# Optimization experiments

Measured on AMD Instinct MI355X. Metric: run time of the kernel, lower is better.

Reference implementation:

```python
import jax, jax.numpy as jnp
import numpy as np

N, E, D_IN, D, L = 50000, 100000, 78, 768, 5
BN_EPS = 1e-5


def setup_inputs() -> dict:
    key = jax.random.key(0)
    ks = jax.random.split(key, 8)
    s_in = 1.0 / np.sqrt(D_IN)
    s_d = 1.0 / np.sqrt(D)
    return {
        "x": jax.random.normal(ks[0], (N, D_IN), dtype=jnp.float32),
        "edge_index": jax.random.randint(ks[1], (2, E), 0, N, dtype=jnp.int32),
        "in_w": jax.random.normal(ks[2], (D_IN, D), dtype=jnp.float32) * s_in,
        "in_b": jnp.zeros((D,), jnp.float32),
        "conv_w": jax.random.normal(ks[3], (L, D, D), dtype=jnp.float32) * s_d,
        "conv_b": jnp.zeros((L, D), jnp.float32),
        "bn_g": jnp.ones((L, D), jnp.float32),
        "bn_b": jnp.zeros((L, D), jnp.float32),
        "out_w": jax.random.normal(ks[4], (D, D), dtype=jnp.float32) * s_d,
        "out_b": jnp.zeros((D,), jnp.float32),
    }


def reference(x, edge_index, in_w, in_b, conv_w, conv_b, bn_g, bn_b, out_w, out_b):
    src, dst = edge_index[0], edge_index[1]
    # GCN symmetric normalization with self-loops: deg over dst (col), +1 for self-loop
    deg = jax.ops.segment_sum(jnp.ones((E,), x.dtype), dst, num_segments=N) + 1.0
    dinv = jax.lax.rsqrt(deg)                      # deg >= 1, always finite
    edge_norm = (dinv[src] * dinv[dst])[:, None]   # [E, 1]
    self_norm = (dinv * dinv)[:, None]             # [N, 1] self-loop coefficient

    h = x @ in_w + in_b                            # input_proj -> [N, D]
    for l in range(L):
        xw = h @ conv_w[l]                         # GCNConv linear
        agg = jax.ops.segment_sum(xw[src] * edge_norm, dst, num_segments=N)
        agg = agg + xw * self_norm + conv_b[l]     # self-loop message + bias
        # BatchNorm1d (training mode: batch stats, biased variance)
        mu = jnp.mean(agg, axis=0)
        var = jnp.mean(jnp.square(agg - mu), axis=0)
        hn = (agg - mu) * jax.lax.rsqrt(var + BN_EPS) * bn_g[l] + bn_b[l]
        h = h + jax.nn.relu(hn)                    # residual (drop_ratio=0)
    return h @ out_w + out_b
```

## Files before the change

kernel.cpp:

```cpp
#include <hip/hip_runtime.h>
#include <hip/hip_bf16.h>
#include <stdint.h>

#define NN 50000
#define EE 100000
#define DD 768
#define MP 50176
#define KIN 96
#define SCB 196

typedef _Float16 half_t;
typedef __attribute__((ext_vector_type(8))) _Float16 v8h;
typedef __attribute__((ext_vector_type(4))) float v4f;

__device__ __forceinline__ void gload16(const half_t* g, half_t* l){
  __builtin_amdgcn_global_load_lds(
      (const __attribute__((address_space(1))) unsigned int*)(g),
      (__attribute__((address_space(3))) unsigned int*)(l),
      16, 0, 0);
}

template<int MODE>
__global__ __launch_bounds__(512, 2)
void gemm256_k(const half_t* __restrict__ A,
               const half_t* __restrict__ Bt,
               int K,
               const float* __restrict__ bias,
               float* __restrict__ o32,
               half_t* __restrict__ o16)
{
  __shared__ __align__(16) half_t lds[3*16384];

  const int nwg = gridDim.x;
  const int q = nwg >> 3, r = nwg & 7;
  const int xcd = blockIdx.x & 7, ii = blockIdx.x >> 3;
  const int L = (xcd < r ? xcd*(q+1) : r*(q+1) + (xcd-r)*q) + ii;
  const int rowb = L / 3, colb = L - rowb*3;
  const int m0 = rowb*256, n0 = colb*256;

  const int t = threadIdx.x, l = t&63, w = t>>6;
  const int wm = w>>2, wn = w&3;

  v4f acc[8][4];
  #pragma unroll
  for (int i=0;i<8;++i)
    #pragma unroll
    for (int j=0;j<4;++j){ v4f z = {0.f,0.f,0.f,0.f}; acc[i][j]=z; }

  const int strip = w*2;
  const int srow  = strip*16 + (l>>2);
  const int sch   = ((l&3) ^ ((l>>2)&3))*8;
  const half_t* Asrc = A  + (size_t)(m0 + srow)*K + sch;
  const half_t* Bsrc = Bt + (size_t)(n0 + srow)*K + sch;

  auto STAGE = [&](int kt2, int b){
    half_t* Ab = lds + b*16384;
    half_t* Bb = Ab + 8192;
    const int ko = kt2*32;
    gload16(Asrc + ko,                    Ab + strip*512);
    gload16(Bsrc + ko,                    Bb + strip*512);
    gload16(Asrc + ko + (size_t)16*K,     Ab + strip*512 + 512);
    gload16(Bsrc + ko + (size_t)16*K,     Bb + strip*512 + 512);
  };

  const int nkt = K/32;
  STAGE(0,0); STAGE(1,1); STAGE(2,2);

  const int ra = l&15;
  const int pc = ((l>>4) ^ (l&3))*8;

  int cb = 0;
  for (int kt=0; kt<nkt; ++kt){
    if (kt < nkt-2)      asm volatile("s_waitcnt vmcnt(8)" ::: "memory");
    else if (kt==nkt-2)  asm volatile("s_waitcnt vmcnt(4)" ::: "memory");
    else                 asm volatile("s_waitcnt vmcnt(0)" ::: "memory");
    __builtin_amdgcn_s_barrier();
    asm volatile("" ::: "memory");

    const half_t* Ab = lds + cb*16384;
    const half_t* Bb = Ab + 8192;
    v8h af[8], bf[4];
    #pragma unroll
    for (int n=0;n<4;++n)
      bf[n] = *(const v8h*)(Bb + (wn*64 + n*16 + ra)*32 + pc);
    #pragma unroll
    for (int m=0;m<8;++m)
      af[m] = *(const v8h*)(Ab + (wm*128 + m*16 + ra)*32 + pc);

    __builtin_amdgcn_s_setprio(1);
    #pragma unroll
    for (int m=0;m<8;++m)
      #pragma unroll
      for (int n=0;n<4;++n)
        acc[m][n] = __builtin_amdgcn_mfma_f32_16x16x32_f16(af[m], bf[n], acc[m][n], 0,0,0);
    __builtin_amdgcn_s_setprio(0);

    asm volatile("" ::: "memory");
    __builtin_amdgcn_s_barrier();
    asm volatile("" ::: "memory");

    if (kt+3 < nkt) STAGE(kt+3, cb);
    cb = (cb==2) ? 0 : cb+1;
  }

  if (MODE==2){
    float bv[4];
    #pragma unroll
    for (int n=0;n<4;++n) bv[n] = bias[n0 + wn*64 + n*16 + ra];
    #pragma unroll
    for (int m=0;m<8;++m){
      #pragma unroll
      for (int rr=0;rr<4;++rr){
        int row = m0 + wm*128 + m*16 + (l>>4)*4 + rr;
        if (row >= NN) continue;
        #pragma unroll
        for (int n=0;n<4;++n){
          int col = n0 + wn*64 + n*16 + ra;
          o32[(size_t)row*DD + col] = acc[m][n][rr] + bv[n];
        }
      }
    }
  } else {
    #pragma unroll
    for (int p=0;p<2;++p){
      __syncthreads();
      if (wm==p){
        #pragma unroll
        for (int m=0;m<8;++m)
          #pragma unroll
          for (int rr=0;rr<4;++rr){
            int rw = m*16 + (l>>4)*4 + rr;
            #pragma unroll
            for (int n=0;n<4;++n){
              int col = wn*64 + n*16 + ra;
              lds[rw*256 + (col ^ ((rw&15)<<3))] = (half_t)acc[m][n][rr];
            }
          }
      }
      __syncthreads();
      #pragma unroll
      for (int g=0; g<8; ++g){
        int rw = (t>>5) + g*16;
        int colB = (t&31)*8;
        v8h hv = *(const v8h*)(lds + rw*256 + (colB ^ ((rw&15)<<3)));
        *(v8h*)(o16 + (size_t)(m0 + p*128 + rw)*DD + n0 + colB) = hv;
      }
    }
  }
}

__global__ __launch_bounds__(256)
void gemm128_k(const half_t* __restrict__ A,
               const half_t* __restrict__ Bt,
               int K,
               const float* __restrict__ bias,
               half_t* __restrict__ o16)
{
  __shared__ __align__(16) half_t smem[128*128];
  half_t* As = smem;
  half_t* Bs = smem + 128*32;
  const int nwg = gridDim.x;
  const int q = nwg >> 3, r = nwg & 7;
  const int xcd = blockIdx.x & 7, ii = blockIdx.x >> 3;
  const int L = (xcd < r ? xcd*(q+1) : r*(q+1) + (xcd-r)*q) + ii;
  const int rowb = L / 6, colb = L - rowb*6;
  const int m0 = rowb*128, n0 = colb*128;

  const int t = threadIdx.x, l = t&63, w = t>>6;
  const int wr = w>>1, wc = w&1;
  v4f acc[4][4];
  #pragma unroll
  for (int i=0;i<4;++i)
    #pragma unroll
    for (int j=0;j<4;++j){ v4f z = {0.f,0.f,0.f,0.f}; acc[i][j]=z; }

  const int nkt = K/32;
  for (int kt=0; kt<nkt; ++kt){
    __syncthreads();
    #pragma unroll
    for (int j=0;j<2;++j){
      int br  = w*32 + j*16;
      int row = br + (l>>2);
      int ch  = (l&3) ^ ((row>>1)&3);
      gload16(A  + (size_t)(m0+row)*K + kt*32 + ch*8, As + br*32);
      gload16(Bt + (size_t)(n0+row)*K + kt*32 + ch*8, Bs + br*32);
    }
    __syncthreads();
    v8h af[4], bf[4];
    #pragma unroll
    for (int m=0;m<4;++m){
      int row = wr*64 + m*16 + (l&15);
      int ch = (l>>4) ^ ((row>>1)&3);
      af[m] = *(const v8h*)(As + row*32 + ch*8);
    }
    #pragma unroll
    for (int n=0;n<4;++n){
      int row = wc*64 + n*16 + (l&15);
      int ch = (l>>4) ^ ((row>>1)&3);
      bf[n] = *(const v8h*)(Bs + row*32 + ch*8);
    }
    #pragma unroll
    for (int m=0;m<4;++m)
      #pragma unroll
      for (int n=0;n<4;++n)
        acc[m][n] = __builtin_amdgcn_mfma_f32_16x16x32_f16(af[m], bf[n], acc[m][n], 0,0,0);
  }

  __syncthreads();
  #pragma unroll
  for (int m=0;m<4;++m){
    #pragma unroll
    for (int rr=0;rr<4;++rr){
      int row = wr*64 + m*16 + (l>>4)*4 + rr;
      #pragma unroll
      for (int n=0;n<4;++n){
        int colL = wc*64 + n*16 + (l&15);
        float v = acc[m][n][rr] + bias[n0+colL];
        int col = colL ^ (((row>>2)&3)<<4);
        smem[row*128 + col] = (half_t)v;
      }
    }
  }
  __syncthreads();
  #pragma unroll
  for (int c=0;c<8;++c){
    int row = c*16 + (t>>4);
    int colBase = (t&15)*8;
    int col = colBase ^ (((row>>2)&3)<<4);
    v8h hv = *(const v8h*)(smem + row*128 + col);
    *(v8h*)(o16 + (size_t)(m0+row)*DD + n0 + colBase) = hv;
  }
}

__global__ void k_count(const int* __restrict__ dst, int* __restrict__ cnt){
  int e = blockIdx.x*256 + threadIdx.x;
  if (e < EE) atomicAdd(&cnt[dst[e]], 1);
}
__global__ void k_dinv(const int* __restrict__ cnt, float* __restrict__ dinv){
  int i = blockIdx.x*256 + threadIdx.x;
  if (i < MP) dinv[i] = (i < NN) ? rsqrtf((float)cnt[i] + 1.0f) : 0.f;
}
__global__ void k_bsum(const int* __restrict__ cnt, int* __restrict__ bsum){
  int i = blockIdx.x*256 + threadIdx.x;
  int v = (i < NN) ? cnt[i] : 0;
  #pragma unroll
  for (int o=1;o<64;o<<=1) v += __shfl_xor(v, o);
  __shared__ int ws_[4];
  if ((threadIdx.x&63)==0) ws_[threadIdx.x>>6] = v;
  __syncthreads();
  if (threadIdx.x==0) bsum[blockIdx.x] = ws_[0]+ws_[1]+ws_[2]+ws_[3];
}
__global__ void k_btop(const int* __restrict__ bsum, int* __restrict__ boff){
  if (threadIdx.x==0){
    int run = 0;
    for (int b=0;b<SCB;++b){ boff[b] = run; run += bsum[b]; }
  }
}
__global__ void k_rowptr(const int* __restrict__ cnt, const int* __restrict__ boff,
                         int* __restrict__ rowptr, int* __restrict__ cursor){
  __shared__ int sh[256];
  int i = blockIdx.x*256 + threadIdx.x;
  int v = (i < NN) ? cnt[i] : 0;
  sh[threadIdx.x] = v; __syncthreads();
  #pragma unroll
  for (int o=1;o<256;o<<=1){
    int add = 0;
    if (threadIdx.x >= o) add = sh[threadIdx.x - o];
    __syncthreads();
    sh[threadIdx.x] += add;
    __syncthreads();
  }
  int excl = sh[threadIdx.x] - v + boff[blockIdx.x];
  if (i <= NN) rowptr[i] = excl;
  if (i < NN)  cursor[i] = excl;
}
__global__ void k_fill(const int* __restrict__ src, const int* __restrict__ dst,
                       const float* __restrict__ dinv, int* __restrict__ cursor,
                       int* __restrict__ ss, float* __restrict__ we){
  int e = blockIdx.x*256 + threadIdx.x;
  if (e < EE){
    int s = src[e], d = dst[e];
    int pos = atomicAdd(&cursor[d], 1);
    ss[pos] = s;
    we[pos] = dinv[s]*dinv[d];
  }
}
__global__ void k_x16(const float* __restrict__ x, half_t* __restrict__ x16){
  int idx = blockIdx.x*256 + threadIdx.x;
  if (idx < MP*KIN){
    int row = idx / KIN, k = idx - row*KIN;
    float v = (row < NN && k < 78) ? x[(size_t)row*78 + k] : 0.f;
    x16[idx] = (half_t)v;
  }
}
__global__ void k_tr(const float* __restrict__ src, half_t* __restrict__ dst, int K, int ldk){
  int idx = blockIdx.x*256 + threadIdx.x;
  if (idx < DD*ldk){
    int n = idx / ldk, k = idx - n*ldk;
    dst[idx] = (k < K) ? (half_t)src[(size_t)k*DD + n] : (half_t)0.f;
  }
}

__global__ __launch_bounds__(256)
void k_gather(const int* __restrict__ rowptr, const int* __restrict__ ss,
              const float* __restrict__ we, const half_t* __restrict__ xw,
              const float* __restrict__ dinv, const float* __restrict__ bias,
              half_t* __restrict__ agg16, float* __restrict__ stats){
  const int t = threadIdx.x;
  const float b0 = bias[t], b1 = bias[t+256], b2 = bias[t+512];
  float s0=0,s1=0,s2=0,q0=0,q1=0,q2=0;
  for (int d = blockIdx.x; d < NN; d += gridDim.x){
    int beg = rowptr[d], end = rowptr[d+1];
    float dv = dinv[d], sn = dv*dv;
    const half_t* xr = xw + (size_t)d*DD;
    float a0 = fmaf(sn, (float)xr[t    ], b0);
    float a1 = fmaf(sn, (float)xr[t+256], b1);
    float a2 = fmaf(sn, (float)xr[t+512], b2);
    for (int e=beg; e<end; ++e){
      int s = ss[e]; float wt = we[e];
      const half_t* xs = xw + (size_t)s*DD;
      a0 = fmaf(wt, (float)xs[t    ], a0);
      a1 = fmaf(wt, (float)xs[t+256], a1);
      a2 = fmaf(wt, (float)xs[t+512], a2);
    }
    half_t* ar = agg16 + (size_t)d*DD;
    ar[t] = (half_t)a0; ar[t+256] = (half_t)a1; ar[t+512] = (half_t)a2;
    s0 += a0; q0 += a0*a0;
    s1 += a1; q1 += a1*a1;
    s2 += a2; q2 += a2*a2;
  }
  atomicAdd(&stats[t],        s0); atomicAdd(&stats[t+256],     s1); atomicAdd(&stats[t+512],     s2);
  atomicAdd(&stats[DD+t],     q0); atomicAdd(&stats[DD+t+256],  q1); atomicAdd(&stats[DD+t+512],  q2);
}

__global__ void k_final(const float* __restrict__ stats, const float* __restrict__ g,
                        const float* __restrict__ b, float* __restrict__ sc, float* __restrict__ sh){
  int t = threadIdx.x;
  #pragma unroll
  for (int j=0;j<3;++j){
    int d = t + j*256;
    float mu  = stats[d]      * (1.0f/NN);
    float msq = stats[DD+d]   * (1.0f/NN);
    float var = msq - mu*mu;
    float rstd = rsqrtf(var + 1e-5f);
    float scale = rstd * g[d];
    sc[d] = scale;
    sh[d] = b[d] - mu*scale;
  }
}
__global__ void k_apply(const half_t* __restrict__ agg16, const float* __restrict__ sc,
                        const float* __restrict__ sh, half_t* __restrict__ h16){
  const int total = NN*DD/8;
  for (int i = blockIdx.x*blockDim.x + threadIdx.x; i < total; i += gridDim.x*blockDim.x){
    size_t base = (size_t)i*8;
    int col = (int)(base % DD);
    v8h a = *(const v8h*)(agg16 + base);
    v8h h = *(const v8h*)(h16 + base);
    v8h o;
    #pragma unroll
    for (int j=0;j<8;++j){
      float v = fmaxf(fmaf((float)a[j], sc[col+j], sh[col+j]), 0.f);
      o[j] = (half_t)((float)h[j] + v);
    }
    *(v8h*)(h16 + base) = o;
  }
}

extern "C" void kernel_launch(void* const* d_in, const int* in_sizes, int n_in,
                              void* d_out, int out_size, void* d_ws, size_t ws_size,
                              hipStream_t stream){
  (void)in_sizes; (void)n_in; (void)out_size; (void)ws_size;
  const float* x      = (const float*)d_in[0];
  const int*   ei     = (const int*)  d_in[1];
  const float* in_w   = (const float*)d_in[2];
  const float* in_b   = (const float*)d_in[3];
  const float* conv_w = (const float*)d_in[4];
  const float* conv_b = (const float*)d_in[5];
  const float* bn_g   = (const float*)d_in[6];
  const float* bn_b   = (const float*)d_in[7];
  const float* out_w  = (const float*)d_in[8];
  const float* out_b  = (const float*)d_in[9];
  float* out = (float*)d_out;
  const int* srcI = ei;
  const int* dstI = ei + EE;

  char* ws = (char*)d_ws; size_t off = 0;
  auto alloc = [&](size_t b)->void*{ void* p = ws + off; off += (b + 255) & ~(size_t)255; return p; };
  half_t* h16  = (half_t*)alloc((size_t)MP*DD*2);
  half_t* xw16 = (half_t*)alloc((size_t)MP*DD*2);
  half_t* agg16= (half_t*)alloc((size_t)NN*DD*2);
  half_t* x16  = (half_t*)alloc((size_t)MP*KIN*2);
  half_t* wT   = (half_t*)alloc((size_t)(DD*KIN + 6*DD*DD)*2);
  float* dinv   = (float*)alloc((size_t)MP*4);
  int*   cnt    = (int*)  alloc((size_t)MP*4);
  int*   rowptr = (int*)  alloc((size_t)(NN+1)*4);
  int*   cursor = (int*)  alloc((size_t)NN*4);
  int*   ssE    = (int*)  alloc((size_t)EE*4);
  float* weE    = (float*)alloc((size_t)EE*4);
  int*   bsum   = (int*)  alloc((size_t)SCB*4);
  int*   boff   = (int*)  alloc((size_t)SCB*4);
  float* stats  = (float*)alloc((size_t)4*DD*4);

  half_t* wTin = wT;
  half_t* wTc  = wT + DD*KIN;
  half_t* wTo  = wTc + 5*DD*DD;

  hipMemsetAsync(cnt, 0, (size_t)MP*4, stream);
  k_count<<<(EE+255)/256,256,0,stream>>>(dstI, cnt);
  k_dinv <<<(MP+255)/256,256,0,stream>>>(cnt, dinv);
  k_bsum <<<SCB,256,0,stream>>>(cnt, bsum);
  k_btop <<<1,64,0,stream>>>(bsum, boff);
  k_rowptr<<<SCB,256,0,stream>>>(cnt, boff, rowptr, cursor);
  k_fill <<<(EE+255)/256,256,0,stream>>>(srcI, dstI, dinv, cursor, ssE, weE);
  k_x16  <<<(MP*KIN+255)/256,256,0,stream>>>(x, x16);
  k_tr   <<<(DD*KIN+255)/256,256,0,stream>>>(in_w, wTin, 78, KIN);
  for (int l = 0; l < 5; ++l)
    k_tr <<<(DD*DD+255)/256,256,0,stream>>>(conv_w + (size_t)l*DD*DD, wTc + (size_t)l*DD*DD, DD, DD);
  k_tr   <<<(DD*DD+255)/256,256,0,stream>>>(out_w, wTo, DD, DD);

  const int NWG1 = (MP/128)*(DD/128);
  gemm128_k<<<NWG1,256,0,stream>>>(x16, wTin, KIN, in_b, h16);

  const int NWG2 = (MP/256)*(DD/256);
  for (int l = 0; l < 5; ++l){
    gemm256_k<1><<<NWG2,512,0,stream>>>(h16, wTc + (size_t)l*DD*DD, DD, nullptr, nullptr, xw16);
    hipMemsetAsync(stats, 0, (size_t)2*DD*4, stream);
    k_gather<<<2048,256,0,stream>>>(rowptr, ssE, weE, xw16, dinv, conv_b + l*DD, agg16, stats);
    k_final<<<1,256,0,stream>>>(stats, bn_g + l*DD, bn_b + l*DD, stats+2*DD, stats+3*DD);
    k_apply<<<2048,256,0,stream>>>(agg16, stats+2*DD, stats+3*DD, h16);
  }

  gemm256_k<2><<<NWG2,512,0,stream>>>(h16, wTo, DD, out_b, out, nullptr);
}
```

Baseline: 1.301 ms.

## Double-buffer LDS fragment loads across MFMA steps in 256-tile GEMM

Restructures the main GEMM loop so each step loads the next k-tile's A/B fragments from LDS into a second register set while MFMAs run on the current set. The loop is fully unrolled with a compile-time K, and it now needs one barrier per iteration instead of two. The LDS swizzle is also changed to a different XOR pattern to reduce bank conflicts. This doubles fragment register use, which risks spills or lower occupancy at 512 threads with 2 blocks per CU, and it hardcodes K=768.

```diff
diff --git a/kernel.cpp b/kernel.cpp
--- a/kernel.cpp
+++ b/kernel.cpp
@@ -24,11 +24,12 @@
 __global__ __launch_bounds__(512, 2)
 void gemm256_k(const half_t* __restrict__ A,
                const half_t* __restrict__ Bt,
-               int K,
                const float* __restrict__ bias,
                float* __restrict__ o32,
                half_t* __restrict__ o16)
 {
+  constexpr int K = 768;
+  constexpr int NKT = 24;
   __shared__ __align__(16) half_t lds[3*16384];
 
   const int nwg = gridDim.x;
@@ -49,7 +50,7 @@
 
   const int strip = w*2;
   const int srow  = strip*16 + (l>>2);
-  const int sch   = ((l&3) ^ ((l>>2)&3))*8;
+  const int sch   = ((l&3) ^ ((l>>3)&3))*8;
   const half_t* Asrc = A  + (size_t)(m0 + srow)*K + sch;
   const half_t* Bsrc = Bt + (size_t)(n0 + srow)*K + sch;
 
@@ -57,51 +58,61 @@
     half_t* Ab = lds + b*16384;
     half_t* Bb = Ab + 8192;
     const int ko = kt2*32;
-    gload16(Asrc + ko,                    Ab + strip*512);
-    gload16(Bsrc + ko,                    Bb + strip*512);
-    gload16(Asrc + ko + (size_t)16*K,     Ab + strip*512 + 512);
-    gload16(Bsrc + ko + (size_t)16*K,     Bb + strip*512 + 512);
+    gload16(Asrc + ko,                Ab + strip*512);
+    gload16(Bsrc + ko,                Bb + strip*512);
+    gload16(Asrc + ko + 16*K,         Ab + strip*512 + 512);
+    gload16(Bsrc + ko + 16*K,         Bb + strip*512 + 512);
   };
 
-  const int nkt = K/32;
+  const int ra = l&15;
+  const int pc = ((l>>4) ^ ((ra>>1)&3))*8;
+
+  v8h af[2][8], bf[2][4];
+
+  #define LOADF(s_, base_) do{                                              \
+    const half_t* Ab_ = lds + (base_);                                      \
+    const half_t* Bb_ = Ab_ + 8192;                                         \
+    _Pragma("unroll")                                                       \
+    for (int n_=0;n_<4;++n_) bf[s_][n_] = *(const v8h*)(Bb_ + (wn*64 + n_*16 + ra)*32 + pc); \
+    _Pragma("unroll")                                                       \
+    for (int m_=0;m_<8;++m_) af[s_][m_] = *(const v8h*)(Ab_ + (wm*128 + m_*16 + ra)*32 + pc); \
+  }while(0)
+
+  #define MFMAS(s_) do{                                                     \
+    __builtin_amdgcn_s_setprio(1);                                          \
+    _Pragma("unroll")                                                       \
+    for (int m_=0;m_<8;++m_)                                                \
+      _Pragma("unroll")                                                     \
+      for (int n_=0;n_<4;++n_)                                              \
+        acc[m_][n_] = __builtin_amdgcn_mfma_f32_16x16x32_f16(af[s_][m_], bf[s_][n_], acc[m_][n_], 0,0,0); \
+    __builtin_amdgcn_s_setprio(0);                                          \
+  }while(0)
+
   STAGE(0,0); STAGE(1,1); STAGE(2,2);
-
-  const int ra = l&15;
-  const int pc = ((l>>4) ^ (l&3))*8;
-
-  int cb = 0;
-  for (int kt=0; kt<nkt; ++kt){
-    if (kt < nkt-2)      asm volatile("s_waitcnt vmcnt(8)" ::: "memory");
-    else if (kt==nkt-2)  asm volatile("s_waitcnt vmcnt(4)" ::: "memory");
-    else                 asm volatile("s_waitcnt vmcnt(0)" ::: "memory");
-    __builtin_amdgcn_s_barrier();
-    asm volatile("" ::: "memory");
-
-    const half_t* Ab = lds + cb*16384;
-    const half_t* Bb = Ab + 8192;
-    v8h af[8], bf[4];
-    #pragma unroll
-    for (int n=0;n<4;++n)
-      bf[n] = *(const v8h*)(Bb + (wn*64 + n*16 + ra)*32 + pc);
-    #pragma unroll
-    for (int m=0;m<8;++m)
-      af[m] = *(const v8h*)(Ab + (wm*128 + m*16 + ra)*32 + pc);
-
-    __builtin_amdgcn_s_setprio(1);
-    #pragma unroll
-    for (int m=0;m<8;++m)
-      #pragma unroll
-      for (int n=0;n<4;++n)
-        acc[m][n] = __builtin_amdgcn_mfma_f32_16x16x32_f16(af[m], bf[n], acc[m][n], 0,0,0);
-    __builtin_amdgcn_s_setprio(0);
-
-    asm volatile("" ::: "memory");
-    __builtin_amdgcn_s_barrier();
-    asm volatile("" ::: "memory");
-
-    if (kt+3 < nkt) STAGE(kt+3, cb);
-    cb = (cb==2) ? 0 : cb+1;
-  }
+  asm volatile("s_waitcnt vmcnt(8)" ::: "memory");
+  __builtin_amdgcn_s_barrier();
+  LOADF(0, 0);
+  asm volatile("s_waitcnt lgkmcnt(0)" ::: "memory");
+  __builtin_amdgcn_sched_barrier(0);
+
+  #pragma unroll
+  for (int i=0;i<NKT;++i){
+    const int cur = i&1, nxt = cur^1;
+    if (i < NKT-1){
+      if (i < NKT-2) asm volatile("s_waitcnt vmcnt(4)" ::: "memory");
+      else           asm volatile("s_waitcnt vmcnt(0)" ::: "memory");
+      __builtin_amdgcn_s_barrier();
+      if (i+3 < NKT) STAGE(i+3, i%3);
+      LOADF(nxt, ((i+1)%3)*16384);
+      MFMAS(cur);
+      asm volatile("s_waitcnt lgkmcnt(0)" ::: "memory");
+      __builtin_amdgcn_sched_barrier(0);
+    } else {
+      MFMAS(cur);
+    }
+  }
+  #undef LOADF
+  #undef MFMAS
 
   if (MODE==2){
     float bv[4];
@@ -423,12 +434,12 @@
 
   const int NWG2 = (MP/256)*(DD/256);
   for (int l = 0; l < 5; ++l){
-    gemm256_k<1><<<NWG2,512,0,stream>>>(h16, wTc + (size_t)l*DD*DD, DD, nullptr, nullptr, xw16);
+    gemm256_k<1><<<NWG2,512,0,stream>>>(h16, wTc + (size_t)l*DD*DD, nullptr, nullptr, xw16);
     hipMemsetAsync(stats, 0, (size_t)2*DD*4, stream);
     k_gather<<<2048,256,0,stream>>>(rowptr, ssE, weE, xw16, dinv, conv_b + l*DD, agg16, stats);
     k_final<<<1,256,0,stream>>>(stats, bn_g + l*DD, bn_b + l*DD, stats+2*DD, stats+3*DD);
     k_apply<<<2048,256,0,stream>>>(agg16, stats+2*DD, stats+3*DD, h16);
   }
 
-  gemm256_k<2><<<NWG2,512,0,stream>>>(h16, wTo, DD, out_b, out, nullptr);
-}
+  gemm256_k<2><<<NWG2,512,0,stream>>>(h16, wTo, out_b, out, nullptr);
+}
```

After: 1.231 ms. 1.06x faster.

## Restructure 256-tile GEMM to double-buffered K=64 stages and unroll gather by two

Applied to the files above, without the earlier changes.

The 768-wide GEMM changes from a triple-buffered K=32 pipeline to a double-buffered K=64 pipeline with K fixed at compile time. The main loop is fully unrolled over 12 steps, and the LDS swizzle is adapted to the 64-element row width. This halves the number of barriers per tile and lets more loads be in flight per stage. The cost is 128KB of LDS per block, which may lower occupancy below the 2 blocks per CU that the launch bounds request. Separately, the edge gather loop is unrolled by two so that two neighbor rows are loaded in parallel.

```diff
diff --git a/kernel.cpp b/kernel.cpp
--- a/kernel.cpp
+++ b/kernel.cpp
@@ -24,12 +24,13 @@
 __global__ __launch_bounds__(512, 2)
 void gemm256_k(const half_t* __restrict__ A,
                const half_t* __restrict__ Bt,
-               int K,
                const float* __restrict__ bias,
                float* __restrict__ o32,
                half_t* __restrict__ o16)
 {
-  __shared__ __align__(16) half_t lds[3*16384];
+  constexpr int K = 768;
+  constexpr int NKT = 12;
+  __shared__ __align__(16) half_t lds[2*32768];
 
   const int nwg = gridDim.x;
   const int q = nwg >> 3, r = nwg & 7;
@@ -47,60 +48,67 @@
     #pragma unroll
     for (int j=0;j<4;++j){ v4f z = {0.f,0.f,0.f,0.f}; acc[i][j]=z; }
 
-  const int strip = w*2;
-  const int srow  = strip*16 + (l>>2);
-  const int sch   = ((l&3) ^ ((l>>2)&3))*8;
-  const half_t* Asrc = A  + (size_t)(m0 + srow)*K + sch;
-  const half_t* Bsrc = Bt + (size_t)(n0 + srow)*K + sch;
-
-  auto STAGE = [&](int kt2, int b){
-    half_t* Ab = lds + b*16384;
-    half_t* Bb = Ab + 8192;
-    const int ko = kt2*32;
-    gload16(Asrc + ko,                    Ab + strip*512);
-    gload16(Bsrc + ko,                    Bb + strip*512);
-    gload16(Asrc + ko + (size_t)16*K,     Ab + strip*512 + 512);
-    gload16(Bsrc + ko + (size_t)16*K,     Bb + strip*512 + 512);
+  const int sr = 8*w + (l>>3);
+  const int sc = ((l&7) ^ ((l>>3)&7))*8;
+  const half_t* Asrc = A  + (size_t)(m0 + sr)*K + sc;
+  const half_t* Bsrc = Bt + (size_t)(n0 + sr)*K + sc;
+  const int ldsbase = w*512;
+
+  auto STAGE = [&](int kt, int b){
+    half_t* Ab = lds + b*32768;
+    half_t* Bb = Ab + 16384;
+    const int ko = kt*64;
+    #pragma unroll
+    for (int j=0;j<4;++j){
+      gload16(Asrc + ko + (size_t)(64*j)*K, Ab + j*4096 + ldsbase);
+      gload16(Bsrc + ko + (size_t)(64*j)*K, Bb + j*4096 + ldsbase);
+    }
   };
 
-  const int nkt = K/32;
-  STAGE(0,0); STAGE(1,1); STAGE(2,2);
-
-  const int ra = l&15;
-  const int pc = ((l>>4) ^ (l&3))*8;
-
-  int cb = 0;
-  for (int kt=0; kt<nkt; ++kt){
-    if (kt < nkt-2)      asm volatile("s_waitcnt vmcnt(8)" ::: "memory");
-    else if (kt==nkt-2)  asm volatile("s_waitcnt vmcnt(4)" ::: "memory");
-    else                 asm volatile("s_waitcnt vmcnt(0)" ::: "memory");
+  const int ra = l&15, hi = l>>4;
+  const int pc0 = (((0 + hi) ^ (ra&7)))*8;
+  const int pc1 = (((4 + hi) ^ (ra&7)))*8;
+
+  STAGE(0, 0);
+
+  #pragma unroll
+  for (int i=0;i<NKT;++i){
+    if (i+1 < NKT){
+      STAGE(i+1, (i+1)&1);
+      asm volatile("s_waitcnt vmcnt(8)" ::: "memory");
+    } else {
+      asm volatile("s_waitcnt vmcnt(0)" ::: "memory");
+    }
     __builtin_amdgcn_s_barrier();
-    asm volatile("" ::: "memory");
-
-    const half_t* Ab = lds + cb*16384;
-    const half_t* Bb = Ab + 8192;
-    v8h af[8], bf[4];
-    #pragma unroll
-    for (int n=0;n<4;++n)
-      bf[n] = *(const v8h*)(Bb + (wn*64 + n*16 + ra)*32 + pc);
-    #pragma unroll
-    for (int m=0;m<8;++m)
-      af[m] = *(const v8h*)(Ab + (wm*128 + m*16 + ra)*32 + pc);
+
+    const half_t* Ab = lds + (i&1)*32768;
+    const half_t* Bb = Ab + 16384;
+    v8h af[8][2], bf[4][2];
+    #pragma unroll
+    for (int n=0;n<4;++n){
+      const half_t* rw_ = Bb + (wn*64 + n*16 + ra)*64;
+      bf[n][0] = *(const v8h*)(rw_ + pc0);
+      bf[n][1] = *(const v8h*)(rw_ + pc1);
+    }
+    #pragma unroll
+    for (int m=0;m<8;++m){
+      const half_t* rw_ = Ab + (wm*128 + m*16 + ra)*64;
+      af[m][0] = *(const v8h*)(rw_ + pc0);
+      af[m][1] = *(const v8h*)(rw_ + pc1);
+    }
 
     __builtin_amdgcn_s_setprio(1);
     #pragma unroll
-    for (int m=0;m<8;++m)
+    for (int ks=0;ks<2;++ks)
       #pragma unroll
-      for (int n=0;n<4;++n)
-        acc[m][n] = __builtin_amdgcn_mfma_f32_16x16x32_f16(af[m], bf[n], acc[m][n], 0,0,0);
+      for (int m=0;m<8;++m)
+        #pragma unroll
+        for (int n=0;n<4;++n)
+          acc[m][n] = __builtin_amdgcn_mfma_f32_16x16x32_f16(af[m][ks], bf[n][ks], acc[m][n], 0,0,0);
     __builtin_amdgcn_s_setprio(0);
 
-    asm volatile("" ::: "memory");
+    asm volatile("s_waitcnt lgkmcnt(0)" ::: "memory");
     __builtin_amdgcn_s_barrier();
-    asm volatile("" ::: "memory");
-
-    if (kt+3 < nkt) STAGE(kt+3, cb);
-    cb = (cb==2) ? 0 : cb+1;
   }
 
   if (MODE==2){
@@ -316,12 +324,24 @@
     float a0 = fmaf(sn, (float)xr[t    ], b0);
     float a1 = fmaf(sn, (float)xr[t+256], b1);
     float a2 = fmaf(sn, (float)xr[t+512], b2);
-    for (int e=beg; e<end; ++e){
-      int s = ss[e]; float wt = we[e];
-      const half_t* xs = xw + (size_t)s*DD;
-      a0 = fmaf(wt, (float)xs[t    ], a0);
-      a1 = fmaf(wt, (float)xs[t+256], a1);
-      a2 = fmaf(wt, (float)xs[t+512], a2);
+    int e = beg;
+    for (; e+1 < end; e += 2){
+      int sA = ss[e], sB = ss[e+1];
+      float wA = we[e], wB = we[e+1];
+      const half_t* xA = xw + (size_t)sA*DD;
+      const half_t* xB = xw + (size_t)sB*DD;
+      float uA0 = (float)xA[t], uA1 = (float)xA[t+256], uA2 = (float)xA[t+512];
+      float uB0 = (float)xB[t], uB1 = (float)xB[t+256], uB2 = (float)xB[t+512];
+      a0 += wA*uA0 + wB*uB0;
+      a1 += wA*uA1 + wB*uB1;
+      a2 += wA*uA2 + wB*uB2;
+    }
+    if (e < end){
+      int sA = ss[e]; float wA = we[e];
+      const half_t* xA = xw + (size_t)sA*DD;
+      a0 = fmaf(wA, (float)xA[t    ], a0);
+      a1 = fmaf(wA, (float)xA[t+256], a1);
+      a2 = fmaf(wA, (float)xA[t+512], a2);
     }
     half_t* ar = agg16 + (size_t)d*DD;
     ar[t] = (half_t)a0; ar[t+256] = (half_t)a1; ar[t+512] = (half_t)a2;
@@ -423,12 +443,12 @@
 
   const int NWG2 = (MP/256)*(DD/256);
   for (int l = 0; l < 5; ++l){
-    gemm256_k<1><<<NWG2,512,0,stream>>>(h16, wTc + (size_t)l*DD*DD, DD, nullptr, nullptr, xw16);
+    gemm256_k<1><<<NWG2,512,0,stream>>>(h16, wTc + (size_t)l*DD*DD, nullptr, nullptr, xw16);
     hipMemsetAsync(stats, 0, (size_t)2*DD*4, stream);
     k_gather<<<2048,256,0,stream>>>(rowptr, ssE, weE, xw16, dinv, conv_b + l*DD, agg16, stats);
     k_final<<<1,256,0,stream>>>(stats, bn_g + l*DD, bn_b + l*DD, stats+2*DD, stats+3*DD);
     k_apply<<<2048,256,0,stream>>>(agg16, stats+2*DD, stats+3*DD, h16);
   }
 
-  gemm256_k<2><<<NWG2,512,0,stream>>>(h16, wTo, DD, out_b, out, nullptr);
-}
+  gemm256_k<2><<<NWG2,512,0,stream>>>(h16, wTo, out_b, out, nullptr);
+}
```

New measurement: 1.388 ms. 1.07x slower.
